# Performance work log

Hardware: AMD Instinct MI355X
Metric: run time of the kernel (lower is better)

Reference implementation:

```python
import jax, jax.numpy as jnp
import numpy as np
from jax import lax

IN_PLANES = 512
GROWTH = 32
PLANES = 4 * GROWTH  # 128
EPS = 1e-5


def setup_inputs() -> dict:
    key = jax.random.key(0)
    ks = jax.random.split(key, 10)
    x = jax.random.normal(ks[0], (128, IN_PLANES, 32, 32), dtype=jnp.float32)
    # bn1 affine params (batch-stat BN, track_running_stats=False)
    gamma1 = jax.random.normal(ks[1], (IN_PLANES,), dtype=jnp.float32) * 0.1 + 1.0
    beta1 = jax.random.normal(ks[2], (IN_PLANES,), dtype=jnp.float32) * 0.1
    # convbn1: 1x1 conv weight + folded BN (running stats)
    w1 = jax.random.normal(ks[3], (PLANES, IN_PLANES, 1, 1), dtype=jnp.float32) * (1.0 / np.sqrt(IN_PLANES))
    gamma2 = jax.random.normal(ks[4], (PLANES,), dtype=jnp.float32) * 0.1 + 1.0
    beta2 = jax.random.normal(ks[5], (PLANES,), dtype=jnp.float32) * 0.1
    mean2 = jax.random.normal(ks[6], (PLANES,), dtype=jnp.float32) * 0.1
    var2 = jax.random.uniform(ks[7], (PLANES,), dtype=jnp.float32, minval=0.5, maxval=1.5)
    # conv2: 3x3 conv, padding 1, no bias
    w2 = jax.random.normal(ks[8], (GROWTH, PLANES, 3, 3), dtype=jnp.float32) * (1.0 / np.sqrt(9 * PLANES))
    return {"x": x, "gamma1": gamma1, "beta1": beta1, "w1": w1,
            "gamma2": gamma2, "beta2": beta2, "mean2": mean2, "var2": var2,
            "w2": w2}


def _bn(h, mean, var, gamma, beta):
    # channel-wise affine normalization, NCHW
    inv = lax.rsqrt(var + EPS)
    scale = (gamma * inv)[None, :, None, None]
    shift = (beta - mean * gamma * inv)[None, :, None, None]
    return h * scale + shift


def reference(x, gamma1, beta1, w1, gamma2, beta2, mean2, var2, w2):
    # bn1: batch statistics (track_running_stats=False)
    mu = jnp.mean(x, axis=(0, 2, 3))
    var = jnp.var(x, axis=(0, 2, 3))  # biased, as torch BN normalization
    h = _bn(x, mu, var, gamma1, beta1)
    h = jax.nn.relu(h)
    # convbn1: 1x1 conv then folded BN (running stats)
    h = lax.conv_general_dilated(h, w1, (1, 1), 'VALID',
                                 dimension_numbers=('NCHW', 'OIHW', 'NCHW'))
    h = _bn(h, mean2, var2, gamma2, beta2)
    h = jax.nn.relu(h)
    # conv2: 3x3, stride 1, pad 1, no bias
    out = lax.conv_general_dilated(h, w2, (1, 1), ((1, 1), (1, 1)),
                                   dimension_numbers=('NCHW', 'OIHW', 'NCHW'))
    # dense concat along channels
    return jnp.concatenate([x, out], axis=1)
```

## Files before the change

kernel.cpp:

```cpp
#include <hip/hip_runtime.h>

#define EPS 1e-5f

typedef __bf16 bf16x8 __attribute__((ext_vector_type(8)));
typedef __bf16 bf16x4 __attribute__((ext_vector_type(4)));
typedef unsigned short ushort8 __attribute__((ext_vector_type(8)));
typedef float f32x4 __attribute__((ext_vector_type(4)));

static __device__ __forceinline__ unsigned short f2bf(float f) {
  unsigned int u = __float_as_uint(f);
  u += 0x7fffu + ((u >> 16) & 1u);
  return (unsigned short)(u >> 16);
}


__global__ void __launch_bounds__(256) k1_kernel(
    const float* __restrict__ x, float* __restrict__ out,
    unsigned short* __restrict__ xbf,
    float* __restrict__ psum, float* __restrict__ psq,
    const float* __restrict__ w1, const float* __restrict__ gamma2,
    const float* __restrict__ beta2, const float* __restrict__ mean2,
    const float* __restrict__ var2, const float* __restrict__ w2,
    unsigned short* __restrict__ w1b, unsigned short* __restrict__ w2b,
    float* __restrict__ bias2) {
  const int t = threadIdx.x;
  if (blockIdx.x >= 4096) {
    int idx = (blockIdx.x - 4096) * 256 + t;
    if (idx < 128 * 512) {
      int oc = idx >> 9;
      float s2 = gamma2[oc] * rsqrtf(var2[oc] + EPS);
      w1b[idx] = f2bf(w1[idx] * s2);
    } else if (idx < 128 * 512 + 32 * 1152) {
      int i2 = idx - 128 * 512;
      int oc = i2 / 1152;
      int rem = i2 - oc * 1152;
      int tap = rem >> 7;
      int c = rem & 127;
      w2b[i2] = f2bf(w2[(oc * 128 + c) * 9 + tap]);
    } else if (idx < 128 * 512 + 32 * 1152 + 128) {
      int oc = idx - (128 * 512 + 32 * 1152);
      float s2 = gamma2[oc] * rsqrtf(var2[oc] + EPS);
      bias2[oc] = beta2[oc] - mean2[oc] * s2;
    }
    return;
  }
  const int c = blockIdx.x & 511;
  const int nq = blockIdx.x >> 9;
  float sum = 0.f, sq = 0.f;
  const f32x4* __restrict__ x4 = (const f32x4*)x;
  f32x4* out4 = (f32x4*)out;
#pragma unroll 4
  for (int i = 0; i < 16; ++i) {
    const int n = nq * 16 + i;
    f32x4 v = __builtin_nontemporal_load(&x4[(((size_t)n * 512 + c) << 8) + t]);
    __builtin_nontemporal_store(v, &out4[(((size_t)n * 544 + c) << 8) + t]);
    bf16x4 bv;
    bv[0] = (__bf16)v[0]; bv[1] = (__bf16)v[1];
    bv[2] = (__bf16)v[2]; bv[3] = (__bf16)v[3];
    *(bf16x4*)(xbf + (((size_t)n * 512 + c) << 10) + t * 4) = bv;
    sum += v[0] + v[1] + v[2] + v[3];
    sq += v[0] * v[0] + v[1] * v[1] + v[2] * v[2] + v[3] * v[3];
  }
  __shared__ float ls[2][4];
  for (int off = 32; off > 0; off >>= 1) {
    sum += __shfl_down(sum, off);
    sq += __shfl_down(sq, off);
  }
  const int w = t >> 6;
  if ((t & 63) == 0) { ls[0][w] = sum; ls[1][w] = sq; }
  __syncthreads();
  if (t == 0) {
    psum[c * 8 + nq] = ls[0][0] + ls[0][1] + ls[0][2] + ls[0][3];
    psq[c * 8 + nq] = ls[1][0] + ls[1][1] + ls[1][2] + ls[1][3];
  }
}

__global__ void __launch_bounds__(256, 2) conv1_kernel(
    const unsigned short* __restrict__ xbf, const unsigned short* __restrict__ w1b,
    const float* __restrict__ psum, const float* __restrict__ psq,
    const float* __restrict__ g1, const float* __restrict__ be1,
    const float* __restrict__ bias2, unsigned short* __restrict__ h2) {
  const int t = threadIdx.x;
  __shared__ float s1s[512], b1s[512];
  for (int cc = t; cc < 512; cc += 256) {
    float S = 0.f, Q = 0.f;
#pragma unroll
    for (int q = 0; q < 8; ++q) { S += psum[cc * 8 + q]; Q += psq[cc * 8 + q]; }
    float mean = S * (1.0f / 131072.0f);
    float var = Q * (1.0f / 131072.0f) - mean * mean;
    float s = g1[cc] * rsqrtf(var + EPS);
    s1s[cc] = s;
    b1s[cc] = be1[cc] - mean * s;
  }
  __syncthreads();

  const int lane = t & 63;
  const int wv = t >> 6;
  const int n = 127 - (blockIdx.x >> 2);
  const int p0w = (blockIdx.x & 3) * 256 + wv * 64;
  const int l15 = lane & 15;
  const int kb = lane >> 4;

  f32x4 acc[8][4];
#pragma unroll
  for (int m = 0; m < 8; ++m)
#pragma unroll
    for (int g = 0; g < 4; ++g) acc[m][g] = (f32x4){0.f, 0.f, 0.f, 0.f};

  const unsigned short* __restrict__ xn = xbf + (size_t)n * 512 * 1024;

  for (int c0 = 0; c0 < 512; c0 += 32) {
    const int cbase = c0 + kb * 8;
    float s1v[8], b1v[8];
#pragma unroll
    for (int j = 0; j < 8; ++j) {
      s1v[j] = s1s[cbase + j];
      b1v[j] = b1s[cbase + j];
    }
    bf16x8 bf[4];
#pragma unroll
    for (int g = 0; g < 4; ++g) {
      const int p = p0w + g * 16 + l15;
      bf16x8 tmp;
#pragma unroll
      for (int j = 0; j < 8; ++j) {
        float xv = (float)*(const __bf16*)(xn + ((size_t)(cbase + j) << 10) + p);
        float a = fmaxf(fmaf(xv, s1v[j], b1v[j]), 0.f);
        tmp[j] = (__bf16)a;
      }
      bf[g] = tmp;
    }
#pragma unroll
    for (int m = 0; m < 8; ++m) {
      bf16x8 af = *(const bf16x8*)(w1b + (size_t)(m * 16 + l15) * 512 + cbase);
#pragma unroll
      for (int g = 0; g < 4; ++g)
        acc[m][g] = __builtin_amdgcn_mfma_f32_16x16x32_bf16(af, bf[g], acc[m][g], 0, 0, 0);
    }
  }

#pragma unroll
  for (int m = 0; m < 8; ++m) {
    const int ocb = m * 16 + kb * 4;
    float bz0 = bias2[ocb + 0], bz1 = bias2[ocb + 1];
    float bz2 = bias2[ocb + 2], bz3 = bias2[ocb + 3];
#pragma unroll
    for (int g = 0; g < 4; ++g) {
      const int p = p0w + g * 16 + l15;
      bf16x4 hv;
      hv[0] = (__bf16)fmaxf(acc[m][g][0] + bz0, 0.f);
      hv[1] = (__bf16)fmaxf(acc[m][g][1] + bz1, 0.f);
      hv[2] = (__bf16)fmaxf(acc[m][g][2] + bz2, 0.f);
      hv[3] = (__bf16)fmaxf(acc[m][g][3] + bz3, 0.f);
      *(bf16x4*)(h2 + ((size_t)n * 1024 + p) * 128 + ocb) = hv;
    }
  }
}

__global__ void __launch_bounds__(256) conv2_kernel(
    const unsigned short* __restrict__ h2, const unsigned short* __restrict__ w2b,
    float* __restrict__ out) {
  const int t = threadIdx.x;
  const int lane = t & 63;
  const int wv = t >> 6;
  const int n = blockIdx.x >> 2;
  const int pbase = (blockIdx.x & 3) * 256 + wv * 64;
  const int l15 = lane & 15;
  const int kb = lane >> 4;

  f32x4 acc[2][4];
#pragma unroll
  for (int m = 0; m < 2; ++m)
#pragma unroll
    for (int g = 0; g < 4; ++g) acc[m][g] = (f32x4){0.f, 0.f, 0.f, 0.f};

  const unsigned short* __restrict__ h2n = h2 + (size_t)n * 1024 * 128;

#pragma unroll
  for (int tap = 0; tap < 9; ++tap) {
    const int dy = tap / 3 - 1;
    const int dx = tap % 3 - 1;
#pragma unroll
    for (int c0 = 0; c0 < 128; c0 += 32) {
      const int cb = c0 + kb * 8;
      bf16x8 af[2];
#pragma unroll
      for (int m = 0; m < 2; ++m)
        af[m] = *(const bf16x8*)(w2b + (size_t)(m * 16 + l15) * 1152 + tap * 128 + cb);
#pragma unroll
      for (int g = 0; g < 4; ++g) {
        const int p = pbase + g * 16 + l15;
        const int y = (p >> 5) & 31;
        const int xx = p & 31;
        const int y2 = y + dy;
        const int x2 = xx + dx;
        bf16x8 bv = __builtin_bit_cast(bf16x8, (ushort8){0, 0, 0, 0, 0, 0, 0, 0});
        if (y2 >= 0 && y2 < 32 && x2 >= 0 && x2 < 32)
          bv = *(const bf16x8*)(h2n + ((size_t)(y2 * 32 + x2)) * 128 + cb);
#pragma unroll
        for (int m = 0; m < 2; ++m)
          acc[m][g] = __builtin_amdgcn_mfma_f32_16x16x32_bf16(af[m], bv, acc[m][g], 0, 0, 0);
      }
    }
  }

#pragma unroll
  for (int m = 0; m < 2; ++m) {
    const int oc = m * 16 + kb * 4;
#pragma unroll
    for (int g = 0; g < 4; ++g) {
      const int p = pbase + g * 16 + l15;
#pragma unroll
      for (int r = 0; r < 4; ++r)
        __builtin_nontemporal_store(
            acc[m][g][r], &out[((size_t)n * 544 + 512 + oc + r) * 1024 + p]);
    }
  }
}

extern "C" void kernel_launch(void* const* d_in, const int* in_sizes, int n_in,
                              void* d_out, int out_size, void* d_ws, size_t ws_size,
                              hipStream_t stream) {
  const float* x = (const float*)d_in[0];
  const float* gamma1 = (const float*)d_in[1];
  const float* beta1 = (const float*)d_in[2];
  const float* w1 = (const float*)d_in[3];
  const float* gamma2 = (const float*)d_in[4];
  const float* beta2 = (const float*)d_in[5];
  const float* mean2 = (const float*)d_in[6];
  const float* var2 = (const float*)d_in[7];
  const float* w2 = (const float*)d_in[8];
  float* out = (float*)d_out;

  char* ws = (char*)d_ws;
  unsigned short* h2 = (unsigned short*)ws;
  unsigned short* xbf = (unsigned short*)(ws + 33554432);
  unsigned short* w1b = (unsigned short*)(ws + 167772160);
  unsigned short* w2b = (unsigned short*)(ws + 167903232);
  float* bias2 = (float*)(ws + 167976960);
  float* psum = (float*)(ws + 167977472);
  float* psq = (float*)(ws + 167993856);

  k1_kernel<<<4512, 256, 0, stream>>>(x, out, xbf, psum, psq,
                                      w1, gamma2, beta2, mean2, var2, w2,
                                      w1b, w2b, bias2);
  conv1_kernel<<<512, 256, 0, stream>>>(xbf, w1b, psum, psq, gamma1, beta1, bias2, h2);
  conv2_kernel<<<512, 256, 0, stream>>>(h2, w2b, out);
}
```

Measured before the change: 200.4 us.

## Transpose bf16 activations to pixel-major layout, add stats reduce kernel, double conv grids

The first kernel now handles one image and a 128-pixel slice per block. It transposes the fp32 input through shared memory into a pixel-major bf16 copy, so conv1 can load 8 contiguous channels with a single vector load instead of eight strided scalar loads. Per-block channel partial sums go into a new reduce kernel that computes the BN scale and shift once, replacing the per-block recomputation in conv1. Conv1 and conv2 use twice as many blocks, each covering half as many pixels. This trades fewer accumulators per wave for more parallelism, at the cost of an extra launch and a shared-memory transpose.

```diff
diff --git a/kernel.cpp b/kernel.cpp
--- a/kernel.cpp
+++ b/kernel.cpp
@@ -24,8 +24,8 @@
     unsigned short* __restrict__ w1b, unsigned short* __restrict__ w2b,
     float* __restrict__ bias2) {
   const int t = threadIdx.x;
-  if (blockIdx.x >= 4096) {
-    int idx = (blockIdx.x - 4096) * 256 + t;
+  if (blockIdx.x >= 1024) {
+    int idx = (blockIdx.x - 1024) * 256 + t;
     if (idx < 128 * 512) {
       int oc = idx >> 9;
       float s2 = gamma2[oc] * rsqrtf(var2[oc] + EPS);
@@ -44,70 +44,136 @@
     }
     return;
   }
-  const int c = blockIdx.x & 511;
-  const int nq = blockIdx.x >> 9;
-  float sum = 0.f, sq = 0.f;
+
+  __shared__ __align__(16) unsigned short tile[128 * 72];
+  __shared__ float red[2][4][64];
+
+  const int n = blockIdx.x >> 3;
+  const int pq = blockIdx.x & 7;
+  const int q = t & 15;
+  const int ph = t >> 4;
+  const int lane = t & 63;
+  const int wv = t >> 6;
+
   const f32x4* __restrict__ x4 = (const f32x4*)x;
   f32x4* out4 = (f32x4*)out;
-#pragma unroll 4
-  for (int i = 0; i < 16; ++i) {
-    const int n = nq * 16 + i;
-    f32x4 v = __builtin_nontemporal_load(&x4[(((size_t)n * 512 + c) << 8) + t]);
-    __builtin_nontemporal_store(v, &out4[(((size_t)n * 544 + c) << 8) + t]);
-    bf16x4 bv;
-    bv[0] = (__bf16)v[0]; bv[1] = (__bf16)v[1];
-    bv[2] = (__bf16)v[2]; bv[3] = (__bf16)v[3];
-    *(bf16x4*)(xbf + (((size_t)n * 512 + c) << 10) + t * 4) = bv;
-    sum += v[0] + v[1] + v[2] + v[3];
-    sq += v[0] * v[0] + v[1] * v[1] + v[2] * v[2] + v[3] * v[3];
+
+  for (int cb = 0; cb < 8; ++cb) {
+    const int c0 = cb * 64 + q * 4;
+    float sum[4] = {0.f, 0.f, 0.f, 0.f}, sq[4] = {0.f, 0.f, 0.f, 0.f};
+#pragma unroll
+    for (int i = 0; i < 2; ++i) {
+      const int px4 = i * 16 + ph;
+      f32x4 v[4];
+#pragma unroll
+      for (int j = 0; j < 4; ++j) {
+        const size_t gi = (((size_t)n * 512 + c0 + j) << 8) + pq * 32 + px4;
+        v[j] = __builtin_nontemporal_load(&x4[gi]);
+        const size_t go = (((size_t)n * 544 + c0 + j) << 8) + pq * 32 + px4;
+        __builtin_nontemporal_store(v[j], &out4[go]);
+        sum[j] += v[j][0] + v[j][1] + v[j][2] + v[j][3];
+        sq[j] += v[j][0] * v[j][0] + v[j][1] * v[j][1] +
+                 v[j][2] * v[j][2] + v[j][3] * v[j][3];
+      }
+#pragma unroll
+      for (int p2 = 0; p2 < 4; ++p2) {
+        bf16x4 bv;
+        bv[0] = (__bf16)v[0][p2];
+        bv[1] = (__bf16)v[1][p2];
+        bv[2] = (__bf16)v[2][p2];
+        bv[3] = (__bf16)v[3][p2];
+        *(bf16x4*)&tile[(size_t)(px4 * 4 + p2) * 72 + q * 4] = bv;
+      }
+    }
+#pragma unroll
+    for (int j = 0; j < 4; ++j) {
+      sum[j] += __shfl_xor(sum[j], 16);
+      sum[j] += __shfl_xor(sum[j], 32);
+      sq[j] += __shfl_xor(sq[j], 16);
+      sq[j] += __shfl_xor(sq[j], 32);
+    }
+    if (lane < 16) {
+#pragma unroll
+      for (int j = 0; j < 4; ++j) {
+        red[0][wv][q * 4 + j] = sum[j];
+        red[1][wv][q * 4 + j] = sq[j];
+      }
+    }
+    __syncthreads();
+#pragma unroll
+    for (int r = 0; r < 4; ++r) {
+      const int sl = r * 256 + t;
+      const int pl = sl >> 3, co = sl & 7;
+      bf16x8 vv = *(const bf16x8*)&tile[(size_t)pl * 72 + co * 8];
+      *(bf16x8*)(xbf + ((size_t)(n * 1024 + pq * 128 + pl)) * 512 + cb * 64 + co * 8) = vv;
+    }
+    if (t < 64) {
+      float S = red[0][0][t] + red[0][1][t] + red[0][2][t] + red[0][3][t];
+      float Q = red[1][0][t] + red[1][1][t] + red[1][2][t] + red[1][3][t];
+      psum[(size_t)(cb * 64 + t) * 1024 + blockIdx.x] = S;
+      psq[(size_t)(cb * 64 + t) * 1024 + blockIdx.x] = Q;
+    }
+    __syncthreads();
+  }
+}
+
+__global__ void __launch_bounds__(256) reduce_kernel(
+    const float* __restrict__ psum, const float* __restrict__ psq,
+    const float* __restrict__ g1, const float* __restrict__ be1,
+    float* __restrict__ s1, float* __restrict__ b1) {
+  const int c = blockIdx.x;
+  const int t = threadIdx.x;
+  float S = 0.f, Q = 0.f;
+#pragma unroll
+  for (int k = 0; k < 4; ++k) {
+    S += psum[(size_t)c * 1024 + k * 256 + t];
+    Q += psq[(size_t)c * 1024 + k * 256 + t];
+  }
+  for (int off = 32; off > 0; off >>= 1) {
+    S += __shfl_down(S, off);
+    Q += __shfl_down(Q, off);
   }
   __shared__ float ls[2][4];
-  for (int off = 32; off > 0; off >>= 1) {
-    sum += __shfl_down(sum, off);
-    sq += __shfl_down(sq, off);
-  }
   const int w = t >> 6;
-  if ((t & 63) == 0) { ls[0][w] = sum; ls[1][w] = sq; }
+  if ((t & 63) == 0) { ls[0][w] = S; ls[1][w] = Q; }
   __syncthreads();
   if (t == 0) {
-    psum[c * 8 + nq] = ls[0][0] + ls[0][1] + ls[0][2] + ls[0][3];
-    psq[c * 8 + nq] = ls[1][0] + ls[1][1] + ls[1][2] + ls[1][3];
-  }
-}
-
-__global__ void __launch_bounds__(256, 2) conv1_kernel(
+    float St = ls[0][0] + ls[0][1] + ls[0][2] + ls[0][3];
+    float Qt = ls[1][0] + ls[1][1] + ls[1][2] + ls[1][3];
+    float mean = St * (1.0f / 131072.0f);
+    float var = Qt * (1.0f / 131072.0f) - mean * mean;
+    float s = g1[c] * rsqrtf(var + EPS);
+    s1[c] = s;
+    b1[c] = be1[c] - mean * s;
+  }
+}
+
+__global__ void __launch_bounds__(256) conv1_kernel(
     const unsigned short* __restrict__ xbf, const unsigned short* __restrict__ w1b,
-    const float* __restrict__ psum, const float* __restrict__ psq,
-    const float* __restrict__ g1, const float* __restrict__ be1,
+    const float* __restrict__ s1, const float* __restrict__ b1,
     const float* __restrict__ bias2, unsigned short* __restrict__ h2) {
   const int t = threadIdx.x;
   __shared__ float s1s[512], b1s[512];
   for (int cc = t; cc < 512; cc += 256) {
-    float S = 0.f, Q = 0.f;
-#pragma unroll
-    for (int q = 0; q < 8; ++q) { S += psum[cc * 8 + q]; Q += psq[cc * 8 + q]; }
-    float mean = S * (1.0f / 131072.0f);
-    float var = Q * (1.0f / 131072.0f) - mean * mean;
-    float s = g1[cc] * rsqrtf(var + EPS);
-    s1s[cc] = s;
-    b1s[cc] = be1[cc] - mean * s;
+    s1s[cc] = s1[cc];
+    b1s[cc] = b1[cc];
   }
   __syncthreads();
 
   const int lane = t & 63;
   const int wv = t >> 6;
-  const int n = 127 - (blockIdx.x >> 2);
-  const int p0w = (blockIdx.x & 3) * 256 + wv * 64;
+  const int n = 127 - (blockIdx.x >> 3);
+  const int p0w = (blockIdx.x & 7) * 128 + wv * 32;
   const int l15 = lane & 15;
   const int kb = lane >> 4;
 
-  f32x4 acc[8][4];
+  f32x4 acc[8][2];
 #pragma unroll
   for (int m = 0; m < 8; ++m)
 #pragma unroll
-    for (int g = 0; g < 4; ++g) acc[m][g] = (f32x4){0.f, 0.f, 0.f, 0.f};
-
-  const unsigned short* __restrict__ xn = xbf + (size_t)n * 512 * 1024;
+    for (int g = 0; g < 2; ++g) acc[m][g] = (f32x4){0.f, 0.f, 0.f, 0.f};
+
+  const unsigned short* __restrict__ xn = xbf + (size_t)n * 1024 * 512;
 
   for (int c0 = 0; c0 < 512; c0 += 32) {
     const int cbase = c0 + kb * 8;
@@ -117,15 +183,15 @@
       s1v[j] = s1s[cbase + j];
       b1v[j] = b1s[cbase + j];
     }
-    bf16x8 bf[4];
-#pragma unroll
-    for (int g = 0; g < 4; ++g) {
+    bf16x8 bf[2];
+#pragma unroll
+    for (int g = 0; g < 2; ++g) {
       const int p = p0w + g * 16 + l15;
+      bf16x8 xv = *(const bf16x8*)(xn + (size_t)p * 512 + cbase);
       bf16x8 tmp;
 #pragma unroll
       for (int j = 0; j < 8; ++j) {
-        float xv = (float)*(const __bf16*)(xn + ((size_t)(cbase + j) << 10) + p);
-        float a = fmaxf(fmaf(xv, s1v[j], b1v[j]), 0.f);
+        float a = fmaxf(fmaf((float)xv[j], s1v[j], b1v[j]), 0.f);
         tmp[j] = (__bf16)a;
       }
       bf[g] = tmp;
@@ -134,7 +200,7 @@
     for (int m = 0; m < 8; ++m) {
       bf16x8 af = *(const bf16x8*)(w1b + (size_t)(m * 16 + l15) * 512 + cbase);
 #pragma unroll
-      for (int g = 0; g < 4; ++g)
+      for (int g = 0; g < 2; ++g)
         acc[m][g] = __builtin_amdgcn_mfma_f32_16x16x32_bf16(af, bf[g], acc[m][g], 0, 0, 0);
     }
   }
@@ -145,7 +211,7 @@
     float bz0 = bias2[ocb + 0], bz1 = bias2[ocb + 1];
     float bz2 = bias2[ocb + 2], bz3 = bias2[ocb + 3];
 #pragma unroll
-    for (int g = 0; g < 4; ++g) {
+    for (int g = 0; g < 2; ++g) {
       const int p = p0w + g * 16 + l15;
       bf16x4 hv;
       hv[0] = (__bf16)fmaxf(acc[m][g][0] + bz0, 0.f);
@@ -163,16 +229,16 @@
   const int t = threadIdx.x;
   const int lane = t & 63;
   const int wv = t >> 6;
-  const int n = blockIdx.x >> 2;
-  const int pbase = (blockIdx.x & 3) * 256 + wv * 64;
+  const int n = blockIdx.x >> 3;
+  const int pbase = (blockIdx.x & 7) * 128 + wv * 32;
   const int l15 = lane & 15;
   const int kb = lane >> 4;
 
-  f32x4 acc[2][4];
+  f32x4 acc[2][2];
 #pragma unroll
   for (int m = 0; m < 2; ++m)
 #pragma unroll
-    for (int g = 0; g < 4; ++g) acc[m][g] = (f32x4){0.f, 0.f, 0.f, 0.f};
+    for (int g = 0; g < 2; ++g) acc[m][g] = (f32x4){0.f, 0.f, 0.f, 0.f};
 
   const unsigned short* __restrict__ h2n = h2 + (size_t)n * 1024 * 128;
 
@@ -188,7 +254,7 @@
       for (int m = 0; m < 2; ++m)
         af[m] = *(const bf16x8*)(w2b + (size_t)(m * 16 + l15) * 1152 + tap * 128 + cb);
 #pragma unroll
-      for (int g = 0; g < 4; ++g) {
+      for (int g = 0; g < 2; ++g) {
         const int p = pbase + g * 16 + l15;
         const int y = (p >> 5) & 31;
         const int xx = p & 31;
@@ -208,7 +274,7 @@
   for (int m = 0; m < 2; ++m) {
     const int oc = m * 16 + kb * 4;
 #pragma unroll
-    for (int g = 0; g < 4; ++g) {
+    for (int g = 0; g < 2; ++g) {
       const int p = pbase + g * 16 + l15;
 #pragma unroll
       for (int r = 0; r < 4; ++r)
@@ -238,12 +304,15 @@
   unsigned short* w1b = (unsigned short*)(ws + 167772160);
   unsigned short* w2b = (unsigned short*)(ws + 167903232);
   float* bias2 = (float*)(ws + 167976960);
-  float* psum = (float*)(ws + 167977472);
-  float* psq = (float*)(ws + 167993856);
-
-  k1_kernel<<<4512, 256, 0, stream>>>(x, out, xbf, psum, psq,
+  float* s1 = (float*)(ws + 167977472);
+  float* b1 = (float*)(ws + 167979520);
+  float* psum = (float*)(ws + 167981568);
+  float* psq = (float*)(ws + 170078720);
+
+  k1_kernel<<<1425, 256, 0, stream>>>(x, out, xbf, psum, psq,
                                       w1, gamma2, beta2, mean2, var2, w2,
                                       w1b, w2b, bias2);
-  conv1_kernel<<<512, 256, 0, stream>>>(xbf, w1b, psum, psq, gamma1, beta1, bias2, h2);
-  conv2_kernel<<<512, 256, 0, stream>>>(h2, w2b, out);
-}
+  reduce_kernel<<<512, 256, 0, stream>>>(psum, psq, gamma1, beta1, s1, b1);
+  conv1_kernel<<<1024, 256, 0, stream>>>(xbf, w1b, s1, b1, bias2, h2);
+  conv2_kernel<<<1024, 256, 0, stream>>>(h2, w2b, out);
+}
```

Result: slower. 307.8 us (+53.6%).

## Fuse input copy and bf16 read into conv1, split conv2 into smaller tiles

Applied to the files above, without the earlier changes.

The first kernel no longer writes the passthrough copy of x or a bf16 staging tensor; it only computes per-channel statistics and prepares the weights. The 1x1 conv kernel now reads fp32 x directly, using register double-buffering to prefetch the next channel chunk. It writes the concat copy into the output while applying BN+ReLU for the MFMA operands. This removes the bf16 staging write and its re-read, but x is now read twice, and conv1 (512 blocks) carries all the copy traffic with strided fp32 loads. The 3x3 conv2 grid also doubles, with each wave covering half the pixels, to raise parallelism.

```diff
diff --git a/kernel.cpp b/kernel.cpp
--- a/kernel.cpp
+++ b/kernel.cpp
@@ -14,9 +14,8 @@
 }
 
 
-__global__ void __launch_bounds__(256) k1_kernel(
-    const float* __restrict__ x, float* __restrict__ out,
-    unsigned short* __restrict__ xbf,
+__global__ void __launch_bounds__(256) stats_kernel(
+    const float* __restrict__ x,
     float* __restrict__ psum, float* __restrict__ psq,
     const float* __restrict__ w1, const float* __restrict__ gamma2,
     const float* __restrict__ beta2, const float* __restrict__ mean2,
@@ -48,16 +47,10 @@
   const int nq = blockIdx.x >> 9;
   float sum = 0.f, sq = 0.f;
   const f32x4* __restrict__ x4 = (const f32x4*)x;
-  f32x4* out4 = (f32x4*)out;
-#pragma unroll 4
+#pragma unroll 8
   for (int i = 0; i < 16; ++i) {
     const int n = nq * 16 + i;
-    f32x4 v = __builtin_nontemporal_load(&x4[(((size_t)n * 512 + c) << 8) + t]);
-    __builtin_nontemporal_store(v, &out4[(((size_t)n * 544 + c) << 8) + t]);
-    bf16x4 bv;
-    bv[0] = (__bf16)v[0]; bv[1] = (__bf16)v[1];
-    bv[2] = (__bf16)v[2]; bv[3] = (__bf16)v[3];
-    *(bf16x4*)(xbf + (((size_t)n * 512 + c) << 10) + t * 4) = bv;
+    f32x4 v = x4[(((size_t)n * 512 + c) << 8) + t];
     sum += v[0] + v[1] + v[2] + v[3];
     sq += v[0] * v[0] + v[1] * v[1] + v[2] * v[2] + v[3] * v[3];
   }
@@ -76,7 +69,8 @@
 }
 
 __global__ void __launch_bounds__(256, 2) conv1_kernel(
-    const unsigned short* __restrict__ xbf, const unsigned short* __restrict__ w1b,
+    const float* __restrict__ x, float* __restrict__ out,
+    const unsigned short* __restrict__ w1b,
     const float* __restrict__ psum, const float* __restrict__ psq,
     const float* __restrict__ g1, const float* __restrict__ be1,
     const float* __restrict__ bias2, unsigned short* __restrict__ h2) {
@@ -85,7 +79,7 @@
   for (int cc = t; cc < 512; cc += 256) {
     float S = 0.f, Q = 0.f;
 #pragma unroll
-    for (int q = 0; q < 8; ++q) { S += psum[cc * 8 + q]; Q += psq[cc * 8 + q]; }
+    for (int qq = 0; qq < 8; ++qq) { S += psum[cc * 8 + qq]; Q += psq[cc * 8 + qq]; }
     float mean = S * (1.0f / 131072.0f);
     float var = Q * (1.0f / 131072.0f) - mean * mean;
     float s = g1[cc] * rsqrtf(var + EPS);
@@ -97,9 +91,10 @@
   const int lane = t & 63;
   const int wv = t >> 6;
   const int n = 127 - (blockIdx.x >> 2);
-  const int p0w = (blockIdx.x & 3) * 256 + wv * 64;
+  const int q = blockIdx.x & 3;
   const int l15 = lane & 15;
   const int kb = lane >> 4;
+  const int p = q * 256 + wv * 64 + l15;
 
   f32x4 acc[8][4];
 #pragma unroll
@@ -107,36 +102,54 @@
 #pragma unroll
     for (int g = 0; g < 4; ++g) acc[m][g] = (f32x4){0.f, 0.f, 0.f, 0.f};
 
-  const unsigned short* __restrict__ xn = xbf + (size_t)n * 512 * 1024;
-
-  for (int c0 = 0; c0 < 512; c0 += 32) {
-    const int cbase = c0 + kb * 8;
-    float s1v[8], b1v[8];
-#pragma unroll
-    for (int j = 0; j < 8; ++j) {
-      s1v[j] = s1s[cbase + j];
-      b1v[j] = b1s[cbase + j];
-    }
+  const float* __restrict__ xn = x + (size_t)n * 524288;
+  float* __restrict__ outn = out + (size_t)n * 544 * 1024;
+
+  float cur[4][8], nxt[4][8];
+#pragma unroll
+  for (int g = 0; g < 4; ++g)
+#pragma unroll
+    for (int j = 0; j < 8; ++j)
+      cur[g][j] = xn[(size_t)(kb * 8 + j) * 1024 + p + g * 16];
+
+  for (int k = 0; k < 16; ++k) {
+    const int cb = k * 32 + kb * 8;
+    if (k < 15) {
+#pragma unroll
+      for (int g = 0; g < 4; ++g)
+#pragma unroll
+        for (int j = 0; j < 8; ++j)
+          nxt[g][j] = xn[(size_t)(cb + 32 + j) * 1024 + p + g * 16];
+    }
+#pragma unroll
+    for (int g = 0; g < 4; ++g)
+#pragma unroll
+      for (int j = 0; j < 8; ++j)
+        __builtin_nontemporal_store(cur[g][j],
+                                    &outn[(size_t)(cb + j) * 1024 + p + g * 16]);
+    float sv[8], bv[8];
+#pragma unroll
+    for (int j = 0; j < 8; ++j) { sv[j] = s1s[cb + j]; bv[j] = b1s[cb + j]; }
     bf16x8 bf[4];
 #pragma unroll
     for (int g = 0; g < 4; ++g) {
-      const int p = p0w + g * 16 + l15;
       bf16x8 tmp;
 #pragma unroll
-      for (int j = 0; j < 8; ++j) {
-        float xv = (float)*(const __bf16*)(xn + ((size_t)(cbase + j) << 10) + p);
-        float a = fmaxf(fmaf(xv, s1v[j], b1v[j]), 0.f);
-        tmp[j] = (__bf16)a;
-      }
+      for (int j = 0; j < 8; ++j)
+        tmp[j] = (__bf16)fmaxf(fmaf(cur[g][j], sv[j], bv[j]), 0.f);
       bf[g] = tmp;
     }
 #pragma unroll
     for (int m = 0; m < 8; ++m) {
-      bf16x8 af = *(const bf16x8*)(w1b + (size_t)(m * 16 + l15) * 512 + cbase);
+      bf16x8 af = *(const bf16x8*)(w1b + (size_t)(m * 16 + l15) * 512 + cb);
 #pragma unroll
       for (int g = 0; g < 4; ++g)
         acc[m][g] = __builtin_amdgcn_mfma_f32_16x16x32_bf16(af, bf[g], acc[m][g], 0, 0, 0);
     }
+#pragma unroll
+    for (int g = 0; g < 4; ++g)
+#pragma unroll
+      for (int j = 0; j < 8; ++j) cur[g][j] = nxt[g][j];
   }
 
 #pragma unroll
@@ -146,13 +159,13 @@
     float bz2 = bias2[ocb + 2], bz3 = bias2[ocb + 3];
 #pragma unroll
     for (int g = 0; g < 4; ++g) {
-      const int p = p0w + g * 16 + l15;
+      const int pp = q * 256 + wv * 64 + g * 16 + l15;
       bf16x4 hv;
       hv[0] = (__bf16)fmaxf(acc[m][g][0] + bz0, 0.f);
       hv[1] = (__bf16)fmaxf(acc[m][g][1] + bz1, 0.f);
       hv[2] = (__bf16)fmaxf(acc[m][g][2] + bz2, 0.f);
       hv[3] = (__bf16)fmaxf(acc[m][g][3] + bz3, 0.f);
-      *(bf16x4*)(h2 + ((size_t)n * 1024 + p) * 128 + ocb) = hv;
+      *(bf16x4*)(h2 + ((size_t)n * 1024 + pp) * 128 + ocb) = hv;
     }
   }
 }
@@ -163,16 +176,16 @@
   const int t = threadIdx.x;
   const int lane = t & 63;
   const int wv = t >> 6;
-  const int n = blockIdx.x >> 2;
-  const int pbase = (blockIdx.x & 3) * 256 + wv * 64;
+  const int n = blockIdx.x >> 3;
+  const int pbase = (blockIdx.x & 7) * 128 + wv * 32;
   const int l15 = lane & 15;
   const int kb = lane >> 4;
 
-  f32x4 acc[2][4];
+  f32x4 acc[2][2];
 #pragma unroll
   for (int m = 0; m < 2; ++m)
 #pragma unroll
-    for (int g = 0; g < 4; ++g) acc[m][g] = (f32x4){0.f, 0.f, 0.f, 0.f};
+    for (int g = 0; g < 2; ++g) acc[m][g] = (f32x4){0.f, 0.f, 0.f, 0.f};
 
   const unsigned short* __restrict__ h2n = h2 + (size_t)n * 1024 * 128;
 
@@ -188,7 +201,7 @@
       for (int m = 0; m < 2; ++m)
         af[m] = *(const bf16x8*)(w2b + (size_t)(m * 16 + l15) * 1152 + tap * 128 + cb);
 #pragma unroll
-      for (int g = 0; g < 4; ++g) {
+      for (int g = 0; g < 2; ++g) {
         const int p = pbase + g * 16 + l15;
         const int y = (p >> 5) & 31;
         const int xx = p & 31;
@@ -208,7 +221,7 @@
   for (int m = 0; m < 2; ++m) {
     const int oc = m * 16 + kb * 4;
 #pragma unroll
-    for (int g = 0; g < 4; ++g) {
+    for (int g = 0; g < 2; ++g) {
       const int p = pbase + g * 16 + l15;
 #pragma unroll
       for (int r = 0; r < 4; ++r)
@@ -234,16 +247,16 @@
 
   char* ws = (char*)d_ws;
   unsigned short* h2 = (unsigned short*)ws;
-  unsigned short* xbf = (unsigned short*)(ws + 33554432);
-  unsigned short* w1b = (unsigned short*)(ws + 167772160);
-  unsigned short* w2b = (unsigned short*)(ws + 167903232);
-  float* bias2 = (float*)(ws + 167976960);
-  float* psum = (float*)(ws + 167977472);
-  float* psq = (float*)(ws + 167993856);
-
-  k1_kernel<<<4512, 256, 0, stream>>>(x, out, xbf, psum, psq,
-                                      w1, gamma2, beta2, mean2, var2, w2,
-                                      w1b, w2b, bias2);
-  conv1_kernel<<<512, 256, 0, stream>>>(xbf, w1b, psum, psq, gamma1, beta1, bias2, h2);
-  conv2_kernel<<<512, 256, 0, stream>>>(h2, w2b, out);
-}
+  unsigned short* w1b = (unsigned short*)(ws + 33554432);
+  unsigned short* w2b = (unsigned short*)(ws + 33685504);
+  float* bias2 = (float*)(ws + 33759232);
+  float* psum = (float*)(ws + 33763840);
+  float* psq = (float*)(ws + 33780224);
+
+  stats_kernel<<<4497, 256, 0, stream>>>(x, psum, psq,
+                                         w1, gamma2, beta2, mean2, var2, w2,
+                                         w1b, w2b, bias2);
+  conv1_kernel<<<512, 256, 0, stream>>>(x, out, w1b, psum, psq,
+                                        gamma1, beta1, bias2, h2);
+  conv2_kernel<<<1024, 256, 0, stream>>>(h2, w2b, out);
+}
```

Result: slower. 305.7 us (+52.5%).
